# Performance work log

Measured on AMD Instinct MI355X. Metric: run time of the kernel, lower is better.

The kernel has to match this reference:

```python
import jax, jax.numpy as jnp
import numpy as np

# init_kwargs baked in as constants
OUTPUT_TYPE = "all"   # one of 'class', 'box', 'all'
CONF = 0.25
RATIO = 0.25
N = 1_000_000
C = 80


def setup_inputs() -> dict:
    key = jax.random.key(0)
    k1, k2 = jax.random.split(key)
    logits = jax.random.normal(k1, (N, C), dtype=jnp.float32)
    boxes = jax.random.uniform(k2, (N, 4), dtype=jnp.float32)
    return {"logits": logits, "boxes": boxes}


def reference(logits, boxes):
    # Number of top rows to consider (rows assumed pre-sorted by confidence).
    n = logits.shape[0]
    k = max(1, int(n * RATIO)) if n > 0 else 0

    # Row-wise max class score over the first k rows: [k]
    scores = jnp.max(logits[:k], axis=1)

    # The torch loop breaks at the FIRST score < conf. Vectorized: keep[i] = 1
    # iff all scores[0..i] >= conf (cumulative AND as a cumprod of 0/1).
    keep = jnp.cumprod((scores >= CONF).astype(logits.dtype))  # [k]

    total = jnp.zeros((), dtype=logits.dtype)
    if OUTPUT_TYPE in ("class", "all"):
        total = total + jnp.sum(keep * scores)
    if OUTPUT_TYPE in ("box", "all"):
        # targets.extend(boxes[i]) sums all 4 coords of each kept row.
        total = total + jnp.sum(keep[:, None] * boxes[:k])
    # If nothing is kept, keep is all zeros and total == 0.0, matching the
    # torch fallback return of tensor(0.0).
    return total
```

## Files before the change

### kernel.cpp

```cpp
#include <hip/hip_runtime.h>
#include <math.h>

#define CONF 0.25f
#define NCLS 80

__global__ void init_kernel(unsigned int* __restrict__ first_fail, unsigned int k) {
    *first_fail = k;
}

__global__ __launch_bounds__(256) void score_kernel(
    const float* __restrict__ logits,
    const float* __restrict__ boxes,
    float* __restrict__ scores,
    float* __restrict__ boxsum,
    unsigned int* __restrict__ first_fail,
    unsigned int k)
{
    const int tid   = threadIdx.x;
    const int lane4 = tid & 3;
    const int grp   = tid >> 2;
    const unsigned int row = blockIdx.x * 64u + (unsigned int)grp;
    if (row >= k) return;

    const float4* rp = (const float4*)(logits + (size_t)row * NCLS);
    float m = -INFINITY;
#pragma unroll
    for (int t = 0; t < 5; ++t) {
        float4 v = rp[lane4 + 4 * t];
        m = fmaxf(m, fmaxf(fmaxf(v.x, v.y), fmaxf(v.z, v.w)));
    }
    m = fmaxf(m, __shfl_xor(m, 1));
    m = fmaxf(m, __shfl_xor(m, 2));

    if (lane4 == 0) {
        scores[row] = m;
        float4 b = ((const float4*)boxes)[row];
        boxsum[row] = (b.x + b.y) + (b.z + b.w);
        if (m < CONF) atomicMin(first_fail, row);
    }
}

__global__ __launch_bounds__(256) void reduce_kernel(
    const float* __restrict__ scores,
    const float* __restrict__ boxsum,
    const unsigned int* __restrict__ first_fail,
    float* __restrict__ partials,
    unsigned int k)
{
    unsigned int j = *first_fail;
    if (j > k) j = k;

    float s = 0.0f;
    const unsigned int stride = gridDim.x * blockDim.x;
    for (unsigned int i = blockIdx.x * blockDim.x + threadIdx.x; i < j; i += stride)
        s += scores[i] + boxsum[i];

#pragma unroll
    for (int o = 32; o > 0; o >>= 1) s += __shfl_down(s, o);

    __shared__ float ls[4];
    const int lane = threadIdx.x & 63;
    const int wid  = threadIdx.x >> 6;
    if (lane == 0) ls[wid] = s;
    __syncthreads();
    if (threadIdx.x == 0)
        partials[blockIdx.x] = (ls[0] + ls[1]) + (ls[2] + ls[3]);
}

__global__ void final_kernel(const float* __restrict__ partials, float* __restrict__ out) {
    float s = partials[threadIdx.x] + partials[threadIdx.x + 64] +
              partials[threadIdx.x + 128] + partials[threadIdx.x + 192];
#pragma unroll
    for (int o = 32; o > 0; o >>= 1) s += __shfl_down(s, o);
    if (threadIdx.x == 0) out[0] = s;
}

extern "C" void kernel_launch(void* const* d_in, const int* in_sizes, int n_in,
                              void* d_out, int out_size, void* d_ws, size_t ws_size,
                              hipStream_t stream) {
    const float* logits = (const float*)d_in[0];
    const float* boxes  = (const float*)d_in[1];
    float* out = (float*)d_out;

    const unsigned int N = (unsigned int)(in_sizes[0] / NCLS);
    unsigned int k = N / 4;
    if (k < 1) k = 1;

    char* ws = (char*)d_ws;
    unsigned int* first_fail = (unsigned int*)ws;
    float* partials = (float*)(ws + 256);
    float* scores   = (float*)(ws + 4096);
    float* boxsum   = (float*)(ws + 4096 + (size_t)k * 4);

    init_kernel<<<1, 1, 0, stream>>>(first_fail, k);

    const unsigned int nb = (k + 63u) / 64u;
    score_kernel<<<nb, 256, 0, stream>>>(logits, boxes, scores, boxsum, first_fail, k);

    reduce_kernel<<<256, 256, 0, stream>>>(scores, boxsum, first_fail, partials, k);

    final_kernel<<<1, 64, 0, stream>>>(partials, out);
}
```

Measured before the change: 371.5 us.

## Fuse per-block partial sums into score kernel and collapse reduction into single combine

The score kernel now sums score plus box-sum per row into a per-block partial and records a per-block first-failing row in shared memory instead of a global atomic. A single-block combine kernel finds the global first failure, adds the full-block partials, and sums the remaining per-row contributions of the partial block. This drops the init kernel, the separate reduce and final kernels and their launches, and avoids rereading two k-length arrays. The cost is an extra block barrier in the score kernel and a serial single-block combine over about 4k block entries.

```diff
diff --git a/kernel.cpp b/kernel.cpp
--- a/kernel.cpp
+++ b/kernel.cpp
@@ -3,76 +3,92 @@
 
 #define CONF 0.25f
 #define NCLS 80
-
-__global__ void init_kernel(unsigned int* __restrict__ first_fail, unsigned int k) {
-    *first_fail = k;
-}
+#define RPB  64
 
 __global__ __launch_bounds__(256) void score_kernel(
     const float* __restrict__ logits,
     const float* __restrict__ boxes,
-    float* __restrict__ scores,
-    float* __restrict__ boxsum,
-    unsigned int* __restrict__ first_fail,
+    float* __restrict__ contrib,
+    float* __restrict__ block_sum,
+    unsigned int* __restrict__ block_minfail,
     unsigned int k)
 {
     const int tid   = threadIdx.x;
     const int lane4 = tid & 3;
     const int grp   = tid >> 2;
-    const unsigned int row = blockIdx.x * 64u + (unsigned int)grp;
-    if (row >= k) return;
+    const unsigned int row = blockIdx.x * RPB + (unsigned int)grp;
 
-    const float4* rp = (const float4*)(logits + (size_t)row * NCLS);
-    float m = -INFINITY;
+    __shared__ float        wsum[4];
+    __shared__ unsigned int minfail;
+    if (tid == 0) minfail = 0xFFFFFFFFu;
+    __syncthreads();
+
+    float c = 0.0f;
+    if (row < k) {
+        const float4* rp = (const float4*)(logits + (size_t)row * NCLS);
+        float m = -INFINITY;
 #pragma unroll
-    for (int t = 0; t < 5; ++t) {
-        float4 v = rp[lane4 + 4 * t];
-        m = fmaxf(m, fmaxf(fmaxf(v.x, v.y), fmaxf(v.z, v.w)));
+        for (int t = 0; t < 5; ++t) {
+            float4 v = rp[lane4 + 4 * t];
+            m = fmaxf(m, fmaxf(fmaxf(v.x, v.y), fmaxf(v.z, v.w)));
+        }
+        m = fmaxf(m, __shfl_xor(m, 1));
+        m = fmaxf(m, __shfl_xor(m, 2));
+        if (lane4 == 0) {
+            float4 b = ((const float4*)boxes)[row];
+            c = m + ((b.x + b.y) + (b.z + b.w));
+            contrib[row] = c;
+            if (m < CONF) atomicMin(&minfail, row);
+        }
     }
-    m = fmaxf(m, __shfl_xor(m, 1));
-    m = fmaxf(m, __shfl_xor(m, 2));
 
-    if (lane4 == 0) {
-        scores[row] = m;
-        float4 b = ((const float4*)boxes)[row];
-        boxsum[row] = (b.x + b.y) + (b.z + b.w);
-        if (m < CONF) atomicMin(first_fail, row);
+    c += __shfl_down(c, 32);
+    c += __shfl_down(c, 16);
+    c += __shfl_down(c, 8);
+    c += __shfl_down(c, 4);
+    const int lane = tid & 63, wid = tid >> 6;
+    if (lane == 0) wsum[wid] = c;
+    __syncthreads();
+    if (tid == 0) {
+        block_sum[blockIdx.x]     = (wsum[0] + wsum[1]) + (wsum[2] + wsum[3]);
+        block_minfail[blockIdx.x] = minfail;
     }
 }
 
-__global__ __launch_bounds__(256) void reduce_kernel(
-    const float* __restrict__ scores,
-    const float* __restrict__ boxsum,
-    const unsigned int* __restrict__ first_fail,
-    float* __restrict__ partials,
-    unsigned int k)
+__global__ __launch_bounds__(256) void combine_kernel(
+    const float* __restrict__ contrib,
+    const float* __restrict__ block_sum,
+    const unsigned int* __restrict__ block_minfail,
+    float* __restrict__ out,
+    unsigned int k, unsigned int nb)
 {
-    unsigned int j = *first_fail;
+    const int tid  = threadIdx.x;
+    const int lane = tid & 63, wid = tid >> 6;
+
+    unsigned int mf = 0xFFFFFFFFu;
+    for (unsigned int b = tid; b < nb; b += 256)
+        mf = min(mf, block_minfail[b]);
+#pragma unroll
+    for (int o = 32; o > 0; o >>= 1) mf = min(mf, __shfl_down(mf, o));
+    __shared__ unsigned int mfs[4];
+    if (lane == 0) mfs[wid] = mf;
+    __syncthreads();
+    unsigned int j = min(min(mfs[0], mfs[1]), min(mfs[2], mfs[3]));
     if (j > k) j = k;
 
+    const unsigned int fullb = j / RPB;
     float s = 0.0f;
-    const unsigned int stride = gridDim.x * blockDim.x;
-    for (unsigned int i = blockIdx.x * blockDim.x + threadIdx.x; i < j; i += stride)
-        s += scores[i] + boxsum[i];
+    for (unsigned int b = tid; b < fullb; b += 256)
+        s += block_sum[b];
+    for (unsigned int i = fullb * RPB + tid; i < j; i += 256)
+        s += contrib[i];
 
 #pragma unroll
     for (int o = 32; o > 0; o >>= 1) s += __shfl_down(s, o);
-
-    __shared__ float ls[4];
-    const int lane = threadIdx.x & 63;
-    const int wid  = threadIdx.x >> 6;
-    if (lane == 0) ls[wid] = s;
+    __shared__ float ss[4];
+    if (lane == 0) ss[wid] = s;
     __syncthreads();
-    if (threadIdx.x == 0)
-        partials[blockIdx.x] = (ls[0] + ls[1]) + (ls[2] + ls[3]);
-}
-
-__global__ void final_kernel(const float* __restrict__ partials, float* __restrict__ out) {
-    float s = partials[threadIdx.x] + partials[threadIdx.x + 64] +
-              partials[threadIdx.x + 128] + partials[threadIdx.x + 192];
-#pragma unroll
-    for (int o = 32; o > 0; o >>= 1) s += __shfl_down(s, o);
-    if (threadIdx.x == 0) out[0] = s;
+    if (tid == 0) out[0] = (ss[0] + ss[1]) + (ss[2] + ss[3]);
 }
 
 extern "C" void kernel_launch(void* const* d_in, const int* in_sizes, int n_in,
@@ -85,19 +101,17 @@
     const unsigned int N = (unsigned int)(in_sizes[0] / NCLS);
     unsigned int k = N / 4;
     if (k < 1) k = 1;
+    const unsigned int nb = (k + RPB - 1) / RPB;
 
     char* ws = (char*)d_ws;
-    unsigned int* first_fail = (unsigned int*)ws;
-    float* partials = (float*)(ws + 256);
-    float* scores   = (float*)(ws + 4096);
-    float* boxsum   = (float*)(ws + 4096 + (size_t)k * 4);
+    size_t off_bs = (((size_t)k * 4) + 255) & ~(size_t)255;
+    size_t off_mf = (off_bs + (size_t)nb * 4 + 255) & ~(size_t)255;
+    float*        contrib       = (float*)ws;
+    float*        block_sum     = (float*)(ws + off_bs);
+    unsigned int* block_minfail = (unsigned int*)(ws + off_mf);
 
-    init_kernel<<<1, 1, 0, stream>>>(first_fail, k);
-
-    const unsigned int nb = (k + 63u) / 64u;
-    score_kernel<<<nb, 256, 0, stream>>>(logits, boxes, scores, boxsum, first_fail, k);
-
-    reduce_kernel<<<256, 256, 0, stream>>>(scores, boxsum, first_fail, partials, k);
-
-    final_kernel<<<1, 64, 0, stream>>>(partials, out);
+    score_kernel<<<nb, 256, 0, stream>>>(logits, boxes, contrib, block_sum,
+                                         block_minfail, k);
+    combine_kernel<<<1, 256, 0, stream>>>(contrib, block_sum, block_minfail,
+                                          out, k, nb);
 }
```

Result: no change. 373.2 us (+0.5%).
